# Performance work log

Measured on AMD Instinct MI355X. Metric: run time of the kernel, lower is better.

The kernel has to match this reference:

```python
import jax, jax.numpy as jnp
import numpy as np

T, B, H, N = 1024, 8, 8, 32  # x dim D = H*N*N = 8192


def setup_inputs() -> dict:
    key = jax.random.key(0)
    x = jax.random.normal(key, (T, B, H * N * N), dtype=jnp.float32)
    S = jnp.zeros((B, H, N, N), dtype=jnp.float32)
    scale = jnp.float32(1.0)  # init_scale
    bias = jnp.float32(2.0)   # init_bias
    return {"x": x, "S": S, "scale": scale, "bias": bias}


def reference(x, S, scale, bias):
    Tt, Bb, D = x.shape
    _, Hh, n, _ = S.shape
    xr = x.reshape(Tt, Bb, Hh, n, n)  # [T,B,H,n,n]

    def step(S_c, A):
        # A: [B,H,n,n]
        k = A.mean(axis=-1)            # mean over dim 2 per head -> [B,H,n]
        v = A.mean(axis=-2)            # mean over dim 1 per head -> [B,H,n]
        A_mean = A.mean(axis=(-1, -2))  # [B,H]
        beta = jax.nn.sigmoid(scale * A_mean + bias)  # [B,H]
        k_norm = k / (jnp.linalg.norm(k, axis=-1, keepdims=True) + 1e-6)
        retrieved = jnp.einsum('bhij,bhj->bhi', S_c, k_norm)
        delta = v - retrieved
        outer = delta[..., :, None] * k_norm[..., None, :]  # [B,H,n,n]
        S_new = jnp.tanh(beta[..., None, None] * S_c + outer)
        Sq = jnp.einsum('bhij,bhj->bhi', S_new, k_norm)     # [B,H,n]
        out = Sq * jax.nn.silu(Sq)                          # [B,H,n]
        return S_new, out.reshape(Bb, Hh * n)

    S_final, output = jax.lax.scan(step, S, xr)  # output: [T,B,H*n]
    return output, S_final
```

## Files before the change

### kernel.cpp

```cpp
#include <hip/hip_runtime.h>
#include <math.h>

#define T_STEPS 1024
#define NBH     64
#define NTILE   65536

static __device__ __forceinline__ float fast_rcp(float x) {
  return __builtin_amdgcn_rcpf(x);
}
static __device__ __forceinline__ float fast_sigmoid(float x) {
  return fast_rcp(1.0f + __expf(-x));
}
static __device__ __forceinline__ float fast_tanh2(float y) {
  return 1.0f - 2.0f * fast_rcp(1.0f + __expf(y));
}

template <int CTRL>
static __device__ __forceinline__ float dpp_add(float x) {
  int y = __builtin_amdgcn_update_dpp(0, __float_as_int(x), CTRL, 0xF, 0xF, true);
  return x + __int_as_float(y);
}

static __device__ __forceinline__ float red16(float x) {
  x = dpp_add<0xB1>(x);
  x = dpp_add<0x4E>(x);
  x = dpp_add<0x141>(x);
  x = dpp_add<0x140>(x);
  return x;
}

__global__ __launch_bounds__(256) void stats_kernel(
    const float* __restrict__ x, const float* __restrict__ scale_p,
    const float* __restrict__ bias_p, float* __restrict__ knT2,
    float* __restrict__ vvT2, float* __restrict__ bbT2) {
  const int tid = threadIdx.x;
  const int l   = tid & 63;
  const int m   = l & 7;
  const int g   = l >> 3;
  const int wib = tid >> 6;
  const int job = blockIdx.x * 4 + wib;
  const int bh  = job >> 6;
  const int t0  = (job & 63) << 4;
  const float sc = scale_p[0], bi = bias_p[0];

  __shared__ float kn_s[4][512];
  __shared__ float vv_s[4][512];
  __shared__ float bb_s[4][16];
  float* ks = kn_s[wib];
  float* vs = vv_s[wib];
  float* bs = bb_s[wib];

  const float4* xp = (const float4*)(x + ((size_t)t0 * 64 + bh) * 1024);
  float4 a0 = xp[l], a1 = xp[l + 64], a2 = xp[l + 128], a3 = xp[l + 192];

  for (int tt = 0; tt < 16; ++tt) {
    float4 b0, b1, b2, b3;
    if (tt < 15) {
      const float4* xn = xp + (size_t)(tt + 1) * 16384;
      b0 = xn[l]; b1 = xn[l + 64]; b2 = xn[l + 128]; b3 = xn[l + 192];
    }

    float r0 = (a0.x + a0.y) + (a0.z + a0.w);
    float r1 = (a1.x + a1.y) + (a1.z + a1.w);
    float r2 = (a2.x + a2.y) + (a2.z + a2.w);
    float r3 = (a3.x + a3.y) + (a3.z + a3.w);
    r0 += __shfl_xor(r0, 1); r1 += __shfl_xor(r1, 1);
    r2 += __shfl_xor(r2, 1); r3 += __shfl_xor(r3, 1);
    r0 += __shfl_xor(r0, 2); r1 += __shfl_xor(r1, 2);
    r2 += __shfl_xor(r2, 2); r3 += __shfl_xor(r3, 2);
    r0 += __shfl_xor(r0, 4); r1 += __shfl_xor(r1, 4);
    r2 += __shfl_xor(r2, 4); r3 += __shfl_xor(r3, 4);

    float c0 = a0.x + a1.x + a2.x + a3.x;
    float c1 = a0.y + a1.y + a2.y + a3.y;
    float c2 = a0.z + a1.z + a2.z + a3.z;
    float c3 = a0.w + a1.w + a2.w + a3.w;
    c0 += __shfl_xor(c0, 8);  c1 += __shfl_xor(c1, 8);
    c2 += __shfl_xor(c2, 8);  c3 += __shfl_xor(c3, 8);
    c0 += __shfl_xor(c0, 16); c1 += __shfl_xor(c1, 16);
    c2 += __shfl_xor(c2, 16); c3 += __shfl_xor(c3, 16);
    c0 += __shfl_xor(c0, 32); c1 += __shfl_xor(c1, 32);
    c2 += __shfl_xor(c2, 32); c3 += __shfl_xor(c3, 32);

    float t1 = (r0 + r1) + (r2 + r3);
    float t2 = (r0 * r0 + r1 * r1) + (r2 * r2 + r3 * r3);
    t1 += __shfl_xor(t1, 8);  t2 += __shfl_xor(t2, 8);
    t1 += __shfl_xor(t1, 16); t2 += __shfl_xor(t2, 16);
    t1 += __shfl_xor(t1, 32); t2 += __shfl_xor(t2, 32);
    const float norm = sqrtf(t2) * (1.0f / 32.0f);
    const float kscl = (1.0f / 32.0f) * fast_rcp(norm + 1e-6f);

    if (m == 0) {
      ks[(g)      * 16 + tt] = r0 * kscl;
      ks[(g + 8)  * 16 + tt] = r1 * kscl;
      ks[(g + 16) * 16 + tt] = r2 * kscl;
      ks[(g + 24) * 16 + tt] = r3 * kscl;
    }
    if (l < 8) {
      vs[(4 * m)     * 16 + tt] = c0 * (1.0f / 16.0f);
      vs[(4 * m + 1) * 16 + tt] = c1 * (1.0f / 16.0f);
      vs[(4 * m + 2) * 16 + tt] = c2 * (1.0f / 16.0f);
      vs[(4 * m + 3) * 16 + tt] = c3 * (1.0f / 16.0f);
    }
    if (l == 0) {
      const float mean = t1 * (1.0f / 1024.0f);
      bs[tt] = 2.0f * fast_sigmoid(sc * mean + bi);
    }

    a0 = b0; a1 = b1; a2 = b2; a3 = b3;
  }

  const size_t rowbase = (size_t)bh * 32 * T_STEPS + t0;
#pragma unroll
  for (int rep = 0; rep < 2; ++rep) {
    const int c = l + rep * 64;
    const int e = c >> 2;
    const int q = c & 3;
    const float4 kv = *(const float4*)&ks[e * 16 + q * 4];
    const float4 vv = *(const float4*)&vs[e * 16 + q * 4];
    *(float4*)(knT2 + rowbase + (size_t)e * T_STEPS + q * 4) = kv;
    *(float4*)(vvT2 + rowbase + (size_t)e * T_STEPS + q * 4) = vv;
  }
  if (l < 4) {
    const float4 bv = *(const float4*)&bs[l * 4];
    *(float4*)(bbT2 + (size_t)bh * T_STEPS + t0 + l * 4) = bv;
  }
}

__global__ __launch_bounds__(256, 1) void scan_kernel(
    const float* __restrict__ S0, const float* __restrict__ knT2,
    const float* __restrict__ vvT2, const float* __restrict__ bbT2,
    float* __restrict__ out, float* __restrict__ Sfin) {
  const int tid  = threadIdx.x;
  const int lane = tid & 63;
  const int g    = lane >> 4;
  const int s    = lane & 15;
  const int w    = blockIdx.x * 4 + (tid >> 6);
  const int bh   = w >> 3;
  const int i    = (w & 7) * 4 + g;
  const int chain = bh * 32 + i;

  const float2 sini = *(const float2*)(S0 + (size_t)bh * 1024 + i * 32 + 2 * s);
  float Sa = sini.x, Sb = sini.y;

  const float* kn0p = knT2 + ((size_t)bh * 32 + 2 * s) * T_STEPS;
  const float* kn1p = kn0p + T_STEPS;
  const float* vp   = vvT2 + ((size_t)bh * 32 + i) * T_STEPS;
  const float* bp   = bbT2 + (size_t)bh * T_STEPS;

  float Ak0[16], Ak1[16], Av[16], Ab[16];
  float Bk0[16], Bk1[16], Bv[16], Bb[16];

#define LOAD_BLK(K0, K1, VV, BE, TOFF)                                    \
  do {                                                                    \
    const int _to = (TOFF);                                               \
    _Pragma("unroll")                                                     \
    for (int qq = 0; qq < 4; ++qq) {                                      \
      *(float4*)&K0[4 * qq] = *(const float4*)(kn0p + _to + 4 * qq);      \
      *(float4*)&K1[4 * qq] = *(const float4*)(kn1p + _to + 4 * qq);      \
      *(float4*)&VV[4 * qq] = *(const float4*)(vp   + _to + 4 * qq);      \
      *(float4*)&BE[4 * qq] = *(const float4*)(bp   + _to + 4 * qq);      \
    }                                                                     \
  } while (0)

#define STEP_BLK(K0, K1, VV, BE, TBASE)                                   \
  do {                                                                    \
    float oacc = 0.0f;                                                    \
    _Pragma("unroll")                                                     \
    for (int u = 0; u < 16; ++u) {                                        \
      const float c0 = K0[u], c1 = K1[u];                                 \
      const float r  = red16(Sa * c0 + Sb * c1);                          \
      const float D2 = fmaf(-2.0f, r, VV[u]);              \
      const float B2 = BE[u];                                             \
      Sa = fast_tanh2(fmaf(B2, Sa, D2 * c0));                             \
      Sb = fast_tanh2(fmaf(B2, Sb, D2 * c1));                             \
      const float qv = red16(Sa * c0 + Sb * c1);                          \
      const float o  = qv * qv * fast_sigmoid(qv);                        \
      oacc = (u == s) ? o : oacc;                                         \
    }                                                                     \
    outp[(size_t)((TBASE) + s) * 2048] = oacc;                            \
  } while (0)

  float* outp = out + chain;

  LOAD_BLK(Ak0, Ak1, Av, Ab, 0);

  for (int t0 = 0; t0 < T_STEPS; t0 += 32) {
    const int tB = t0 + 16;
    const int tA2 = (t0 + 32 < T_STEPS) ? t0 + 32 : t0;
    LOAD_BLK(Bk0, Bk1, Bv, Bb, tB);
    STEP_BLK(Ak0, Ak1, Av, Ab, t0);
    LOAD_BLK(Ak0, Ak1, Av, Ab, tA2);
    STEP_BLK(Bk0, Bk1, Bv, Bb, tB);
  }

#undef LOAD_BLK
#undef STEP_BLK

  float2 sfin; sfin.x = Sa; sfin.y = Sb;
  *(float2*)(Sfin + (size_t)bh * 1024 + i * 32 + 2 * s) = sfin;
}

extern "C" void kernel_launch(void* const* d_in, const int* in_sizes, int n_in,
                              void* d_out, int out_size, void* d_ws, size_t ws_size,
                              hipStream_t stream) {
  const float* x     = (const float*)d_in[0];
  const float* S0    = (const float*)d_in[1];
  const float* scale = (const float*)d_in[2];
  const float* bias  = (const float*)d_in[3];
  float* out = (float*)d_out;

  float* knT2 = (float*)d_ws;
  float* vvT2 = knT2 + (size_t)NTILE * 32;
  float* bbT2 = vvT2 + (size_t)NTILE * 32;

  stats_kernel<<<1024, 256, 0, stream>>>(x, scale, bias, knT2, vvT2, bbT2);

  float* Sfin = out + (size_t)T_STEPS * 2048;
  scan_kernel<<<128, 256, 0, stream>>>(S0, knT2, vvT2, bbT2, out, Sfin);
}
```

Measured before the change: 465.8 us.

## Fuse stats and scan kernels into producer/consumer kernel with flag sync

Merges the stats and scan kernels into a single launch. Producer blocks compute per-chunk k/v/beta statistics in time-major job order and publish a flag per job. Consumer blocks spin on those flags and run the recurrent scan while later chunks are still being produced, so the memory-bound stats pass overlaps with the latency-bound scan. It relies on all consumer and producer blocks being co-resident, adds a memset launch and spin-wait overhead, and halves the consumer prefetch block size to 8 steps.

After: 1.486 ms. +219.0%, slower.

```diff
diff --git a/kernel.cpp b/kernel.cpp
--- a/kernel.cpp
+++ b/kernel.cpp
@@ -4,6 +4,11 @@
 #define T_STEPS 1024
 #define NBH     64
 #define NTILE   65536
+#define NJOBS   4096
+#define MAGIC   0x13579BDFu
+#define NCONS   128
+#define NPROD   384
+#define PWAVES  (NPROD * 4)
 
 static __device__ __forceinline__ float fast_rcp(float x) {
   return __builtin_amdgcn_rcpf(x);
@@ -29,176 +34,194 @@
   return x;
 }
 
-__global__ __launch_bounds__(256) void stats_kernel(
-    const float* __restrict__ x, const float* __restrict__ scale_p,
-    const float* __restrict__ bias_p, float* __restrict__ knT2,
-    float* __restrict__ vvT2, float* __restrict__ bbT2) {
+__global__ __launch_bounds__(256, 4) void fused_kernel(
+    const float* __restrict__ x, const float* __restrict__ S0,
+    const float* __restrict__ scale_p, const float* __restrict__ bias_p,
+    float* __restrict__ knT2, float* __restrict__ vvT2,
+    float* __restrict__ bbT2, unsigned int* __restrict__ flags,
+    float* __restrict__ out, float* __restrict__ Sfin) {
   const int tid = threadIdx.x;
+  const int wib = tid >> 6;
   const int l   = tid & 63;
-  const int m   = l & 7;
-  const int g   = l >> 3;
-  const int wib = tid >> 6;
-  const int job = blockIdx.x * 4 + wib;
-  const int bh  = job >> 6;
-  const int t0  = (job & 63) << 4;
-  const float sc = scale_p[0], bi = bias_p[0];
 
   __shared__ float kn_s[4][512];
   __shared__ float vv_s[4][512];
   __shared__ float bb_s[4][16];
-  float* ks = kn_s[wib];
-  float* vs = vv_s[wib];
-  float* bs = bb_s[wib];
-
-  const float4* xp = (const float4*)(x + ((size_t)t0 * 64 + bh) * 1024);
-  float4 a0 = xp[l], a1 = xp[l + 64], a2 = xp[l + 128], a3 = xp[l + 192];
-
-  for (int tt = 0; tt < 16; ++tt) {
-    float4 b0, b1, b2, b3;
-    if (tt < 15) {
-      const float4* xn = xp + (size_t)(tt + 1) * 16384;
-      b0 = xn[l]; b1 = xn[l + 64]; b2 = xn[l + 128]; b3 = xn[l + 192];
+
+  if (blockIdx.x >= NCONS) {
+    const int m = l & 7;
+    const int g = l >> 3;
+    const float sc = scale_p[0], bi = bias_p[0];
+    float* ks = kn_s[wib];
+    float* vs = vv_s[wib];
+    float* bs = bb_s[wib];
+    const int pw = (blockIdx.x - NCONS) * 4 + wib;
+
+    for (int job = pw; job < NJOBS; job += PWAVES) {
+      const int bh = job & 63;
+      const int t0 = (job >> 6) << 4;
+
+      const float4* xp = (const float4*)(x + ((size_t)t0 * 64 + bh) * 1024);
+      float4 a0 = xp[l], a1 = xp[l + 64], a2 = xp[l + 128], a3 = xp[l + 192];
+
+      for (int tt = 0; tt < 16; ++tt) {
+        float4 b0, b1, b2, b3;
+        if (tt < 15) {
+          const float4* xn = xp + (size_t)(tt + 1) * 16384;
+          b0 = xn[l]; b1 = xn[l + 64]; b2 = xn[l + 128]; b3 = xn[l + 192];
+        }
+
+        float r0 = (a0.x + a0.y) + (a0.z + a0.w);
+        float r1 = (a1.x + a1.y) + (a1.z + a1.w);
+        float r2 = (a2.x + a2.y) + (a2.z + a2.w);
+        float r3 = (a3.x + a3.y) + (a3.z + a3.w);
+        r0 += __shfl_xor(r0, 1); r1 += __shfl_xor(r1, 1);
+        r2 += __shfl_xor(r2, 1); r3 += __shfl_xor(r3, 1);
+        r0 += __shfl_xor(r0, 2); r1 += __shfl_xor(r1, 2);
+        r2 += __shfl_xor(r2, 2); r3 += __shfl_xor(r3, 2);
+        r0 += __shfl_xor(r0, 4); r1 += __shfl_xor(r1, 4);
+        r2 += __shfl_xor(r2, 4); r3 += __shfl_xor(r3, 4);
+
+        float c0 = a0.x + a1.x + a2.x + a3.x;
+        float c1 = a0.y + a1.y + a2.y + a3.y;
+        float c2 = a0.z + a1.z + a2.z + a3.z;
+        float c3 = a0.w + a1.w + a2.w + a3.w;
+        c0 += __shfl_xor(c0, 8);  c1 += __shfl_xor(c1, 8);
+        c2 += __shfl_xor(c2, 8);  c3 += __shfl_xor(c3, 8);
+        c0 += __shfl_xor(c0, 16); c1 += __shfl_xor(c1, 16);
+        c2 += __shfl_xor(c2, 16); c3 += __shfl_xor(c3, 16);
+        c0 += __shfl_xor(c0, 32); c1 += __shfl_xor(c1, 32);
+        c2 += __shfl_xor(c2, 32); c3 += __shfl_xor(c3, 32);
+
+        float t1 = (r0 + r1) + (r2 + r3);
+        float t2 = (r0 * r0 + r1 * r1) + (r2 * r2 + r3 * r3);
+        t1 += __shfl_xor(t1, 8);  t2 += __shfl_xor(t2, 8);
+        t1 += __shfl_xor(t1, 16); t2 += __shfl_xor(t2, 16);
+        t1 += __shfl_xor(t1, 32); t2 += __shfl_xor(t2, 32);
+        const float norm = sqrtf(t2) * (1.0f / 32.0f);
+        const float kscl = (1.0f / 32.0f) * fast_rcp(norm + 1e-6f);
+
+        if (m == 0) {
+          ks[(g)      * 16 + tt] = r0 * kscl;
+          ks[(g + 8)  * 16 + tt] = r1 * kscl;
+          ks[(g + 16) * 16 + tt] = r2 * kscl;
+          ks[(g + 24) * 16 + tt] = r3 * kscl;
+        }
+        if (l < 8) {
+          vs[(4 * m)     * 16 + tt] = c0 * (1.0f / 16.0f);
+          vs[(4 * m + 1) * 16 + tt] = c1 * (1.0f / 16.0f);
+          vs[(4 * m + 2) * 16 + tt] = c2 * (1.0f / 16.0f);
+          vs[(4 * m + 3) * 16 + tt] = c3 * (1.0f / 16.0f);
+        }
+        if (l == 0) {
+          const float mean = t1 * (1.0f / 1024.0f);
+          bs[tt] = 2.0f * fast_sigmoid(sc * mean + bi);
+        }
+
+        a0 = b0; a1 = b1; a2 = b2; a3 = b3;
+      }
+
+      const size_t rowbase = (size_t)bh * 32 * T_STEPS + t0;
+#pragma unroll
+      for (int rep = 0; rep < 2; ++rep) {
+        const int c = l + rep * 64;
+        const int e = c >> 2;
+        const int q = c & 3;
+        const float4 kv = *(const float4*)&ks[e * 16 + q * 4];
+        const float4 vq = *(const float4*)&vs[e * 16 + q * 4];
+        *(float4*)(knT2 + rowbase + (size_t)e * T_STEPS + q * 4) = kv;
+        *(float4*)(vvT2 + rowbase + (size_t)e * T_STEPS + q * 4) = vq;
+      }
+      if (l < 4) {
+        const float4 bv = *(const float4*)&bs[l * 4];
+        *(float4*)(bbT2 + (size_t)bh * T_STEPS + t0 + l * 4) = bv;
+      }
+
+      __threadfence();
+      if (l == 0) atomicExch(&flags[job], MAGIC);
     }
-
-    float r0 = (a0.x + a0.y) + (a0.z + a0.w);
-    float r1 = (a1.x + a1.y) + (a1.z + a1.w);
-    float r2 = (a2.x + a2.y) + (a2.z + a2.w);
-    float r3 = (a3.x + a3.y) + (a3.z + a3.w);
-    r0 += __shfl_xor(r0, 1); r1 += __shfl_xor(r1, 1);
-    r2 += __shfl_xor(r2, 1); r3 += __shfl_xor(r3, 1);
-    r0 += __shfl_xor(r0, 2); r1 += __shfl_xor(r1, 2);
-    r2 += __shfl_xor(r2, 2); r3 += __shfl_xor(r3, 2);
-    r0 += __shfl_xor(r0, 4); r1 += __shfl_xor(r1, 4);
-    r2 += __shfl_xor(r2, 4); r3 += __shfl_xor(r3, 4);
-
-    float c0 = a0.x + a1.x + a2.x + a3.x;
-    float c1 = a0.y + a1.y + a2.y + a3.y;
-    float c2 = a0.z + a1.z + a2.z + a3.z;
-    float c3 = a0.w + a1.w + a2.w + a3.w;
-    c0 += __shfl_xor(c0, 8);  c1 += __shfl_xor(c1, 8);
-    c2 += __shfl_xor(c2, 8);  c3 += __shfl_xor(c3, 8);
-    c0 += __shfl_xor(c0, 16); c1 += __shfl_xor(c1, 16);
-    c2 += __shfl_xor(c2, 16); c3 += __shfl_xor(c3, 16);
-    c0 += __shfl_xor(c0, 32); c1 += __shfl_xor(c1, 32);
-    c2 += __shfl_xor(c2, 32); c3 += __shfl_xor(c3, 32);
-
-    float t1 = (r0 + r1) + (r2 + r3);
-    float t2 = (r0 * r0 + r1 * r1) + (r2 * r2 + r3 * r3);
-    t1 += __shfl_xor(t1, 8);  t2 += __shfl_xor(t2, 8);
-    t1 += __shfl_xor(t1, 16); t2 += __shfl_xor(t2, 16);
-    t1 += __shfl_xor(t1, 32); t2 += __shfl_xor(t2, 32);
-    const float norm = sqrtf(t2) * (1.0f / 32.0f);
-    const float kscl = (1.0f / 32.0f) * fast_rcp(norm + 1e-6f);
-
-    if (m == 0) {
-      ks[(g)      * 16 + tt] = r0 * kscl;
-      ks[(g + 8)  * 16 + tt] = r1 * kscl;
-      ks[(g + 16) * 16 + tt] = r2 * kscl;
-      ks[(g + 24) * 16 + tt] = r3 * kscl;
-    }
-    if (l < 8) {
-      vs[(4 * m)     * 16 + tt] = c0 * (1.0f / 16.0f);
-      vs[(4 * m + 1) * 16 + tt] = c1 * (1.0f / 16.0f);
-      vs[(4 * m + 2) * 16 + tt] = c2 * (1.0f / 16.0f);
-      vs[(4 * m + 3) * 16 + tt] = c3 * (1.0f / 16.0f);
-    }
-    if (l == 0) {
-      const float mean = t1 * (1.0f / 1024.0f);
-      bs[tt] = 2.0f * fast_sigmoid(sc * mean + bi);
-    }
-
-    a0 = b0; a1 = b1; a2 = b2; a3 = b3;
-  }
-
-  const size_t rowbase = (size_t)bh * 32 * T_STEPS + t0;
-#pragma unroll
-  for (int rep = 0; rep < 2; ++rep) {
-    const int c = l + rep * 64;
-    const int e = c >> 2;
-    const int q = c & 3;
-    const float4 kv = *(const float4*)&ks[e * 16 + q * 4];
-    const float4 vv = *(const float4*)&vs[e * 16 + q * 4];
-    *(float4*)(knT2 + rowbase + (size_t)e * T_STEPS + q * 4) = kv;
-    *(float4*)(vvT2 + rowbase + (size_t)e * T_STEPS + q * 4) = vv;
-  }
-  if (l < 4) {
-    const float4 bv = *(const float4*)&bs[l * 4];
-    *(float4*)(bbT2 + (size_t)bh * T_STEPS + t0 + l * 4) = bv;
-  }
-}
-
-__global__ __launch_bounds__(256, 1) void scan_kernel(
-    const float* __restrict__ S0, const float* __restrict__ knT2,
-    const float* __restrict__ vvT2, const float* __restrict__ bbT2,
-    float* __restrict__ out, float* __restrict__ Sfin) {
-  const int tid  = threadIdx.x;
-  const int lane = tid & 63;
-  const int g    = lane >> 4;
-  const int s    = lane & 15;
-  const int w    = blockIdx.x * 4 + (tid >> 6);
-  const int bh   = w >> 3;
-  const int i    = (w & 7) * 4 + g;
-  const int chain = bh * 32 + i;
-
-  const float2 sini = *(const float2*)(S0 + (size_t)bh * 1024 + i * 32 + 2 * s);
-  float Sa = sini.x, Sb = sini.y;
-
-  const float* kn0p = knT2 + ((size_t)bh * 32 + 2 * s) * T_STEPS;
-  const float* kn1p = kn0p + T_STEPS;
-  const float* vp   = vvT2 + ((size_t)bh * 32 + i) * T_STEPS;
-  const float* bp   = bbT2 + (size_t)bh * T_STEPS;
-
-  float Ak0[16], Ak1[16], Av[16], Ab[16];
-  float Bk0[16], Bk1[16], Bv[16], Bb[16];
-
-#define LOAD_BLK(K0, K1, VV, BE, TOFF)                                    \
+  } else {
+    const int g = l >> 4;
+    const int s = l & 15;
+    const int w = blockIdx.x * 4 + wib;
+    const int bh = w >> 3;
+    const int i  = (w & 7) * 4 + g;
+    const int chain = bh * 32 + i;
+
+    const float2 sini =
+        *(const float2*)(S0 + (size_t)bh * 1024 + i * 32 + 2 * s);
+    float Sa = sini.x, Sb = sini.y;
+
+    const float* kn0p = knT2 + ((size_t)bh * 32 + 2 * s) * T_STEPS;
+    const float* kn1p = kn0p + T_STEPS;
+    const float* vp   = vvT2 + ((size_t)bh * 32 + i) * T_STEPS;
+    const float* bp   = bbT2 + (size_t)bh * T_STEPS;
+    float* outp = out + chain;
+
+    float ak0[8], ak1[8], av[8], ab[8];
+    float bk0[8], bk1[8], bv[8], bbuf[8];
+
+#define WAITC(c)                                                          \
   do {                                                                    \
-    const int _to = (TOFF);                                               \
+    if (l == 0) {                                                         \
+      while (atomicOr(&flags[(size_t)(c)*64 + bh], 0u) != MAGIC)          \
+        __builtin_amdgcn_s_sleep(16);                                     \
+    }                                                                     \
+    __threadfence();                            \
+  } while (0)
+
+#define LOADSB(K0, K1, VV, BE, sb)                                        \
+  do {                                                                    \
+    const int _t = (sb)*8;                                                \
+    *(float4*)&K0[0] = *(const float4*)(kn0p + _t);                       \
+    *(float4*)&K0[4] = *(const float4*)(kn0p + _t + 4);                   \
+    *(float4*)&K1[0] = *(const float4*)(kn1p + _t);                       \
+    *(float4*)&K1[4] = *(const float4*)(kn1p + _t + 4);                   \
+    *(float4*)&VV[0] = *(const float4*)(vp + _t);                         \
+    *(float4*)&VV[4] = *(const float4*)(vp + _t + 4);                     \
+    *(float4*)&BE[0] = *(const float4*)(bp + _t);                         \
+    *(float4*)&BE[4] = *(const float4*)(bp + _t + 4);                     \
+  } while (0)
+
+#define COMPUTE8(K0, K1, VV, BE, OFF)                                     \
+  do {                                                                    \
     _Pragma("unroll")                                                     \
-    for (int qq = 0; qq < 4; ++qq) {                                      \
-      *(float4*)&K0[4 * qq] = *(const float4*)(kn0p + _to + 4 * qq);      \
-      *(float4*)&K1[4 * qq] = *(const float4*)(kn1p + _to + 4 * qq);      \
-      *(float4*)&VV[4 * qq] = *(const float4*)(vp   + _to + 4 * qq);      \
-      *(float4*)&BE[4 * qq] = *(const float4*)(bp   + _to + 4 * qq);      \
-    }                                                                     \
-  } while (0)
-
-#define STEP_BLK(K0, K1, VV, BE, TBASE)                                   \
-  do {                                                                    \
-    float oacc = 0.0f;                                                    \
-    _Pragma("unroll")                                                     \
-    for (int u = 0; u < 16; ++u) {                                        \
+    for (int u = 0; u < 8; ++u) {                                         \
       const float c0 = K0[u], c1 = K1[u];                                 \
       const float r  = red16(Sa * c0 + Sb * c1);                          \
-      const float D2 = fmaf(-2.0f, r, VV[u]);              \
+      const float D2 = fmaf(-2.0f, r, VV[u]);                             \
       const float B2 = BE[u];                                             \
       Sa = fast_tanh2(fmaf(B2, Sa, D2 * c0));                             \
       Sb = fast_tanh2(fmaf(B2, Sb, D2 * c1));                             \
       const float qv = red16(Sa * c0 + Sb * c1);                          \
       const float o  = qv * qv * fast_sigmoid(qv);                        \
-      oacc = (u == s) ? o : oacc;                                         \
+      oacc = ((u + (OFF)) == s) ? o : oacc;                               \
     }                                                                     \
-    outp[(size_t)((TBASE) + s) * 2048] = oacc;                            \
   } while (0)
 
-  float* outp = out + chain;
-
-  LOAD_BLK(Ak0, Ak1, Av, Ab, 0);
-
-  for (int t0 = 0; t0 < T_STEPS; t0 += 32) {
-    const int tB = t0 + 16;
-    const int tA2 = (t0 + 32 < T_STEPS) ? t0 + 32 : t0;
-    LOAD_BLK(Bk0, Bk1, Bv, Bb, tB);
-    STEP_BLK(Ak0, Ak1, Av, Ab, t0);
-    LOAD_BLK(Ak0, Ak1, Av, Ab, tA2);
-    STEP_BLK(Bk0, Bk1, Bv, Bb, tB);
+    WAITC(0);
+    LOADSB(ak0, ak1, av, ab, 0);
+    LOADSB(bk0, bk1, bv, bbuf, 1);
+    float oacc = 0.0f;
+
+    for (int c = 0; c < 64; ++c) {
+      COMPUTE8(ak0, ak1, av, ab, 0);
+      if (c < 63) {
+        WAITC(c + 1);
+        LOADSB(ak0, ak1, av, ab, 2 * c + 2);
+      }
+      COMPUTE8(bk0, bk1, bv, bbuf, 8);
+      outp[(size_t)(c * 16 + s) * 2048] = oacc;
+      if (c < 63) LOADSB(bk0, bk1, bv, bbuf, 2 * c + 3);
+    }
+
+#undef WAITC
+#undef LOADSB
+#undef COMPUTE8
+
+    float2 sfin; sfin.x = Sa; sfin.y = Sb;
+    *(float2*)(Sfin + (size_t)bh * 1024 + i * 32 + 2 * s) = sfin;
   }
-
-#undef LOAD_BLK
-#undef STEP_BLK
-
-  float2 sfin; sfin.x = Sa; sfin.y = Sb;
-  *(float2*)(Sfin + (size_t)bh * 1024 + i * 32 + 2 * s) = sfin;
 }
 
 extern "C" void kernel_launch(void* const* d_in, const int* in_sizes, int n_in,
@@ -213,9 +236,11 @@
   float* knT2 = (float*)d_ws;
   float* vvT2 = knT2 + (size_t)NTILE * 32;
   float* bbT2 = vvT2 + (size_t)NTILE * 32;
-
-  stats_kernel<<<1024, 256, 0, stream>>>(x, scale, bias, knT2, vvT2, bbT2);
+  unsigned int* flags = (unsigned int*)(bbT2 + (size_t)NBH * T_STEPS);
+
+  hipMemsetAsync(flags, 0, NJOBS * sizeof(unsigned int), stream);
 
   float* Sfin = out + (size_t)T_STEPS * 2048;
-  scan_kernel<<<128, 256, 0, stream>>>(S0, knT2, vvT2, bbT2, out, Sfin);
-}
+  fused_kernel<<<NCONS + NPROD, 256, 0, stream>>>(
+      x, S0, scale, bias, knT2, vvT2, bbT2, flags, out, Sfin);
+}
```
